# Kernel optimization log

Measured on AMD Instinct MI355X. Metric: run time of the kernel, lower is better.

Reference implementation:

```python
import math
import jax, jax.numpy as jnp
import numpy as np

L, B = 576, 16           # residues, batch
HID, ALPHA = 800, 60     # lstm hidden, alphabet size
IN0, IN1 = 41, 2 * HID   # lstm layer input sizes (20 one-hot + 21 pssm)


def _unit(v):
    return v / jnp.linalg.norm(v, axis=-1, keepdims=True)


def _frame(a, b, c):
    # rotation matrix (columns) of the local reference frame at point c
    bc = _unit(c - b)
    n = _unit(jnp.cross(b - a, bc))
    return jnp.stack([bc, jnp.cross(n, bc), n], axis=-1)  # (..., 3, 3)


def _extend(a, b, c, ct):
    # place next atom given previous three atoms and SRF coordinates ct
    R = _frame(a, b, c)
    return c + jnp.einsum('...ij,...j->...i', R, ct)


def lstm_dir(x, w_ih, w_hh, b_ih, b_hh, reverse=False):
    # single-direction LSTM over x: (T, B, D); torch gate order i,f,g,o
    H = w_hh.shape[1]
    Bb = x.shape[1]

    def step(carry, xt):
        h, cst = carry
        gates = xt @ w_ih.T + b_ih + h @ w_hh.T + b_hh
        i, f, g, o = jnp.split(gates, 4, axis=-1)
        cnew = jax.nn.sigmoid(f) * cst + jax.nn.sigmoid(i) * jnp.tanh(g)
        hnew = jax.nn.sigmoid(o) * jnp.tanh(cnew)
        return (hnew, cnew), hnew

    zeros = jnp.zeros((Bb, H), x.dtype)
    _, hs = jax.lax.scan(step, (zeros, zeros), x, reverse=reverse)
    return hs  # (T, B, H), in original time order for both directions


def torsion_to_srf(r, theta, phi):
    # r, theta: (3,) fixed bond lengths/angles; phi: (L, B, 3) torsions
    r = r[None, None, :]
    th = theta[None, None, :]
    c = jnp.stack([r * jnp.cos(th) * jnp.ones_like(phi),
                   r * jnp.cos(phi) * jnp.sin(th),
                   r * jnp.sin(phi) * jnp.sin(th)], axis=-1)  # (L, B, 3, 3)
    Lx, Bx = phi.shape[0], phi.shape[1]
    return jnp.transpose(c, (0, 2, 1, 3)).reshape(3 * Lx, Bx, 3)


def pnerf(c_tilde, nfrag):
    # parallel NeRF: run nfrag fragments in parallel, then stitch sequentially
    A, Bb, _ = c_tilde.shape
    F = A // nfrag  # assumes divisibility (guaranteed by chosen L)
    c = c_tilde.reshape(nfrag, F, Bb, 3).transpose(1, 0, 2, 3).reshape(F, nfrag * Bb, 3)
    init = jnp.array([[-np.sqrt(0.5), np.sqrt(1.5), 0.0],
                      [-np.sqrt(2.0), 0.0, 0.0],
                      [0.0, 0.0, 0.0]], dtype=c_tilde.dtype)
    a0 = jnp.broadcast_to(init[0], (nfrag * Bb, 3))
    b0 = jnp.broadcast_to(init[1], (nfrag * Bb, 3))
    c0 = jnp.broadcast_to(init[2], (nfrag * Bb, 3))

    def step(carry, ct):
        a, b, cc = carry
        d = _extend(a, b, cc, ct)
        return (b, cc, d), d

    _, frag = jax.lax.scan(step, (a0, b0, c0), c)  # (F, nfrag*Bb, 3)
    frag = frag.reshape(F, nfrag, Bb, 3)

    coords = frag[:, 0]  # fragment 0 already in global frame
    for k in range(1, nfrag):  # small fixed loop over fragments
        R = _frame(coords[-3], coords[-2], coords[-1])  # (Bb, 3, 3)
        g = coords[-1][None] + jnp.einsum('bij,fbj->fbi', R, frag[:, k])
        coords = jnp.concatenate([coords, g], axis=0)
    return coords  # (3L, B, 3)


def _p(k, shape):
    return 0.05 * jax.random.normal(k, shape, dtype=jnp.float32)


def setup_inputs():
    key = jax.random.key(0)
    ks = jax.random.split(key, 32)
    inp = {}
    inp['seq'] = jax.random.randint(ks[0], (L, B), 0, 20)
    inp['pssm'] = jax.random.uniform(ks[1], (L, B, 21), dtype=jnp.float32)
    inp['length'] = jnp.full((B,), L, dtype=jnp.int32)  # full lengths (packing is a no-op)
    i = 2
    for layer, din in ((0, IN0), (1, IN1)):
        for d in ('f', 'b'):
            inp[f'w_ih_l{layer}{d}'] = _p(ks[i], (4 * HID, din)); i += 1
            inp[f'w_hh_l{layer}{d}'] = _p(ks[i], (4 * HID, HID)); i += 1
            inp[f'b_ih_l{layer}{d}'] = _p(ks[i], (4 * HID,)); i += 1
            inp[f'b_hh_l{layer}{d}'] = _p(ks[i], (4 * HID,)); i += 1
    inp['fc_w'] = _p(ks[i], (ALPHA, 2 * HID)); i += 1
    inp['fc_b'] = _p(ks[i], (ALPHA,)); i += 1
    inp['alphabet'] = jax.random.uniform(ks[i], (ALPHA, 3), minval=-math.pi, maxval=math.pi, dtype=jnp.float32); i += 1
    inp['bond_lengths'] = jnp.array([145.867432, 152.534744, 132.935516], dtype=jnp.float32)
    inp['bond_angles'] = jnp.array([1.019982, 1.20471, 1.109421], dtype=jnp.float32)
    return inp


def reference(seq, pssm, length,
              w_ih_l0f, w_hh_l0f, b_ih_l0f, b_hh_l0f,
              w_ih_l0b, w_hh_l0b, b_ih_l0b, b_hh_l0b,
              w_ih_l1f, w_hh_l1f, b_ih_l1f, b_hh_l1f,
              w_ih_l1b, w_hh_l1b, b_ih_l1b, b_hh_l1b,
              fc_w, fc_b, alphabet, bond_lengths, bond_angles):
    # eval mode: inter-layer dropout omitted; all lengths == L so packing is identity
    x = jnp.concatenate([jax.nn.one_hot(seq, 20, dtype=pssm.dtype), pssm], axis=-1)  # (L,B,41)
    h = jnp.concatenate([lstm_dir(x, w_ih_l0f, w_hh_l0f, b_ih_l0f, b_hh_l0f),
                         lstm_dir(x, w_ih_l0b, w_hh_l0b, b_ih_l0b, b_hh_l0b, reverse=True)], axis=-1)
    h = jnp.concatenate([lstm_dir(h, w_ih_l1f, w_hh_l1f, b_ih_l1f, b_hh_l1f),
                         lstm_dir(h, w_ih_l1b, w_hh_l1b, b_ih_l1b, b_hh_l1b, reverse=True)], axis=-1)
    p = jax.nn.softmax(h @ fc_w.T + fc_b, axis=-1)            # (L,B,ALPHA)
    phi = jnp.arctan2(p @ jnp.sin(alphabet), p @ jnp.cos(alphabet))  # (L,B,3)
    srf = torsion_to_srf(bond_lengths, bond_angles, phi)      # (3L,B,3)
    return pnerf(srf, int(math.sqrt(L)))                      # (3L,B,3)
```

## Files before the change

### kernel.cpp

```cpp
#include <hip/hip_runtime.h>
#include <hip/hip_fp16.h>

#define L_SEQ 576
#define BATCH 16
#define HIDDEN 800
#define NT 200
#define KQ_HH 25
#define KQ_L1 50
#define KQ_L0 2

typedef _Float16 h8 __attribute__((ext_vector_type(8)));
typedef _Float16 h4 __attribute__((ext_vector_type(4)));
typedef float f4 __attribute__((ext_vector_type(4)));
typedef int v4i __attribute__((ext_vector_type(4)));
typedef int v2i __attribute__((ext_vector_type(2)));

__device__ __forceinline__ float sigmoidf_(float x){
  x = fminf(30.f, fmaxf(-30.f, x));
  return 1.f/(1.f+__expf(-x));
}
__device__ __forceinline__ float tanhf_(float x){
  x = fminf(15.f, fmaxf(-15.f, x));
  float e = __expf(2.f*x);
  return (e-1.f)/(e+1.f);
}

__global__ void init_h(v4i* __restrict__ h){
  size_t i = (size_t)blockIdx.x*256 + threadIdx.x;
  v4i s = {0x7C007C00, 0x7C007C00, 0x7C007C00, 0x7C007C00};
  h[i] = s;
}

__global__ void build_x(const int* __restrict__ seq, const float* __restrict__ pssm,
                        _Float16* __restrict__ x){
  int i = blockIdx.x*256 + threadIdx.x;
  if(i >= L_SEQ*BATCH*64) return;
  int m = i >> 6, k = i & 63;
  float v = 0.f;
  if(k < 20)      v = (seq[m]==k) ? 1.f : 0.f;
  else if(k < 41) v = pssm[m*21 + (k-20)];
  x[i] = (_Float16)v;
}

__global__ void prep_w(
  const float* __restrict__ whh0f, const float* __restrict__ whh0b,
  const float* __restrict__ whh1f, const float* __restrict__ whh1b,
  const float* __restrict__ wih1f, const float* __restrict__ wih1b,
  const float* __restrict__ wih0f, const float* __restrict__ wih0b,
  h8* __restrict__ wp_hh, h8* __restrict__ wp1, h8* __restrict__ wp0)
{
  long idx = (long)blockIdx.x*256 + threadIdx.x;
  const long J1 = 4L*320000, J2 = 2L*640000, J3 = 2L*25600;
  if(idx < J1){
    int d = (int)(idx/320000); int r = (int)(idx%320000);
    int T = r/1600, q = (r%1600)/64, l = r&63;
    const float* W = (d==0)?whh0f:(d==1)?whh0b:(d==2)?whh1f:whh1b;
    int c = l&15; int n = (c&3)*800 + T*4 + (c>>2);
    const float* src = W + (size_t)n*800 + q*32 + ((l>>4)<<3);
    h8 v;
    #pragma unroll
    for(int j=0;j<8;++j) v[j] = (_Float16)src[j];
    wp_hh[idx] = v;
  } else if(idx < J1+J2){
    long i2 = idx - J1;
    int d = (int)(i2/640000); int r = (int)(i2%640000);
    int T = r/3200, q = (r%3200)/64, l = r&63;
    const float* W = d ? wih1b : wih1f;
    int c = l&15; int n = (c&3)*800 + T*4 + (c>>2);
    const float* src = W + (size_t)n*1600 + q*32 + ((l>>4)<<3);
    h8 v;
    #pragma unroll
    for(int j=0;j<8;++j) v[j] = (_Float16)src[j];
    wp1[i2] = v;
  } else if(idx < J1+J2+J3){
    long i3 = idx - J1 - J2;
    int d = (int)(i3/25600); int r = (int)(i3%25600);
    int T = r/128, q = (r%128)/64, l = r&63;
    const float* W = d ? wih0b : wih0f;
    int c = l&15; int n = (c&3)*800 + T*4 + (c>>2);
    int k0 = q*32 + ((l>>4)<<3);
    h8 v;
    #pragma unroll
    for(int j=0;j<8;++j){ int k = k0+j; v[j] = (_Float16)((k<41)? W[(size_t)n*41+k] : 0.f); }
    wp0[i3] = v;
  }
}

__global__ __launch_bounds__(256) void gemm_l0(
  const _Float16* __restrict__ A,
  const h8* __restrict__ WpF, const h8* __restrict__ WpB,
  const float* __restrict__ bihF, const float* __restrict__ bhhF,
  const float* __restrict__ bihB, const float* __restrict__ bhhB,
  _Float16* __restrict__ GpF, _Float16* __restrict__ GpB)
{
  const int wv = threadIdx.x >> 6;
  const int l  = threadIdx.x & 63;
  const int mg = blockIdx.x % 144;
  const int tg = blockIdx.x / 144;
  const int mt = mg*4 + wv;
  const int dir = tg / 50;
  const int Tb  = (tg % 50) * 4;
  const h8* Wp = dir ? WpB : WpF;
  const float* bih = dir ? bihB : bihF;
  const float* bhh = dir ? bhhB : bhhF;
  _Float16* Gp = dir ? GpB : GpF;

  const _Float16* ab = A + (size_t)(mt*16 + (l&15))*64 + ((l>>4)<<3);
  f4 acc[4] = {{0.f,0.f,0.f,0.f},{0.f,0.f,0.f,0.f},{0.f,0.f,0.f,0.f},{0.f,0.f,0.f,0.f}};
  for(int q=0;q<KQ_L0;++q){
    h8 av = *(const h8*)(ab + q*32);
    #pragma unroll
    for(int j=0;j<4;++j){
      h8 bv = Wp[((size_t)(Tb+j)*KQ_L0 + q)*64 + l];
      acc[j] = __builtin_amdgcn_mfma_f32_16x16x32_f16(bv, av, acc[j], 0, 0, 0);
    }
  }
  const int hi = l >> 4;
  #pragma unroll
  for(int j=0;j<4;++j){
    int T = Tb + j;
    int u = T*4 + hi;
    h4 o;
    #pragma unroll
    for(int r=0;r<4;++r){
      float bias = bih[r*800+u] + bhh[r*800+u];
      o[r] = (_Float16)(acc[j][r] + bias);
    }
    *(h4*)(Gp + (((size_t)mt*NT + T)*64 + l)*4) = o;
  }
}

__global__ __launch_bounds__(256,1) void lstm_kernel(
  const h8* __restrict__ WpF, const h8* __restrict__ WpB,
  const _Float16* __restrict__ GpF, const _Float16* __restrict__ GpB,
  h8* __restrict__ hfrag)
{
  __shared__ __attribute__((aligned(16))) char lds_h[2*25600];
  const int tid = threadIdx.x;
  const int wv  = tid >> 6;
  const int l   = tid & 63;
  const bool bwd = blockIdx.x >= 50;
  const int T = ((bwd ? (int)blockIdx.x - 50 : (int)blockIdx.x) << 2) + wv;
  const h8* Wp = bwd ? WpB : WpF;
  const _Float16* Gp = bwd ? GpB : GpF;
  const int dirOff = bwd ? 1600 : 0;

  h8 Bf[KQ_HH];
  #pragma unroll
  for(int q=0;q<KQ_HH;++q) Bf[q] = Wp[(T*KQ_HH + q)*64 + l];

  float cs = 0.f;
  const int qb = wv*6;
  const int storeUnit = ((T>>3)<<6) + (((T>>1)&3)<<4);
  const int storeHalf = (T&1)<<3;

  for(int s=0; s<L_SEQ; ++s){
    const int t = bwd ? (L_SEQ-1-s) : s;

    h4 gp4 = *(const h4*)(Gp + (((size_t)t*NT + T)*64 + l)*4);

    #pragma unroll
    for(int q=0;q<KQ_HH;++q) asm volatile("" : "+v"(Bf[q]));

    char* lbuf = lds_h + (s&1)*25600;
    if(s > 0){
      const h8* src = hfrag + (size_t)(bwd ? t+1 : t-1)*3200 + dirOff + l;
      v4i w[7];
      for(;;){
        #pragma unroll
        for(int i=0;i<7;++i){
          unsigned long long ad = (unsigned long long)(src + (qb+i)*64);
          asm volatile("global_load_dwordx4 %0, %1, off sc1"
                       : "=v"(w[i]) : "v"(ad) : "memory");
        }
        asm volatile("s_waitcnt vmcnt(0)"
          : "+v"(w[0]),"+v"(w[1]),"+v"(w[2]),"+v"(w[3]),"+v"(w[4]),
            "+v"(w[5]),"+v"(w[6])
          :
          : "memory");
        int orac = 0;
        #pragma unroll
        for(int i=0;i<7;++i) orac |= (w[i][0]|w[i][1]) | (w[i][2]|w[i][3]);
        if(__all((orac & 0x40004000) == 0)) break;
        __builtin_amdgcn_s_sleep(1);
      }
      #pragma unroll
      for(int i=0;i<7;++i)
        *(v4i*)(lbuf + (qb+i)*1024 + l*16) = w[i];
    }
    __syncthreads();

    f4 acc[4];
    acc[0][0]=(float)gp4[0]; acc[0][1]=(float)gp4[1]; acc[0][2]=(float)gp4[2]; acc[0][3]=(float)gp4[3];
    #pragma unroll
    for(int j=1;j<4;++j){ acc[j][0]=0.f; acc[j][1]=0.f; acc[j][2]=0.f; acc[j][3]=0.f; }
    if(s > 0){
      #pragma unroll
      for(int q=0;q<KQ_HH;++q){
        v4i wq = *(const v4i*)(lbuf + q*1024 + l*16);
        acc[q&3] = __builtin_amdgcn_mfma_f32_16x16x32_f16(
                     Bf[q], __builtin_bit_cast(h8, wq), acc[q&3], 0,0,0);
      }
    }
    f4 g = (acc[0]+acc[1]) + (acc[2]+acc[3]);

    float cn = sigmoidf_(g[1])*cs + sigmoidf_(g[0])*tanhf_(g[2]);
    cs = cn;
    float hv = sigmoidf_(g[3])*tanhf_(cn);

    {
      _Float16 hf = (_Float16)hv;
      unsigned int u0 = (unsigned int)__builtin_bit_cast(unsigned short, hf);
      unsigned int up = (unsigned int)__shfl_xor((int)u0, 16, 64);
      unsigned int d01 = u0 | (up << 16);
      unsigned int d23 = (unsigned int)__shfl_xor((int)d01, 32, 64);
      if(l < 16){
        v2i ov; ov[0] = (int)d01; ov[1] = (int)d23;
        unsigned long long ad = (unsigned long long)
          ((char*)(hfrag + (size_t)t*3200 + dirOff + storeUnit + l) + storeHalf);
        asm volatile("global_store_dwordx2 %0, %1, off sc1" : : "v"(ad), "v"(ov) : "memory");
      }
    }
  }
}

__global__ __launch_bounds__(512,1) void fused_l1(
  const h8* __restrict__ WhF, const h8* __restrict__ WhB,
  _Float16* __restrict__ GpF, _Float16* __restrict__ GpB,
  h8* __restrict__ hfrag,
  const h8* __restrict__ Af,
  const h8* __restrict__ W1F, const h8* __restrict__ W1B,
  const float* __restrict__ bihF, const float* __restrict__ bhhF,
  const float* __restrict__ bihB, const float* __restrict__ bhhB)
{
  __shared__ __attribute__((aligned(16))) char smem[2*25600];
  const int tid = threadIdx.x;
  if(blockIdx.x < 100){
    const bool act = tid < 256;
    const int wv = (tid >> 6) & 3;
    const int l  = tid & 63;
    const bool bwd = blockIdx.x >= 50;
    const int T = ((bwd ? (int)blockIdx.x - 50 : (int)blockIdx.x) << 2) + wv;
    const h8* Wp = bwd ? WhB : WhF;
    const _Float16* Gp = bwd ? GpB : GpF;
    const int dirOff = bwd ? 1600 : 0;

    h8 Bf[KQ_HH];
    if(act){
      #pragma unroll
      for(int q=0;q<KQ_HH;++q) Bf[q] = Wp[(T*KQ_HH + q)*64 + l];
    }
    float cs = 0.f;
    const int qb = wv*6;
    const int storeUnit = ((T>>3)<<6) + (((T>>1)&3)<<4);
    const int storeHalf = (T&1)<<3;

    for(int s=0; s<L_SEQ; ++s){
      const int t = bwd ? (L_SEQ-1-s) : s;
      v2i gpw;
      char* lbuf = smem + (s&1)*25600;
      unsigned long long gpad = 0;
      if(act){
        gpad = (unsigned long long)(Gp + (((size_t)t*NT + T)*64 + l)*4);
        asm volatile("global_load_dwordx2 %0, %1, off sc1"
                     : "=v"(gpw) : "v"(gpad) : "memory");
        #pragma unroll
        for(int q=0;q<KQ_HH;++q) asm volatile("" : "+v"(Bf[q]));
        if(s > 0){
          const h8* src = hfrag + (size_t)(bwd ? t+1 : t-1)*3200 + dirOff + l;
          v4i w[7];
          for(;;){
            #pragma unroll
            for(int i=0;i<7;++i){
              unsigned long long ad = (unsigned long long)(src + (qb+i)*64);
              asm volatile("global_load_dwordx4 %0, %1, off sc1"
                           : "=v"(w[i]) : "v"(ad) : "memory");
            }
            asm volatile("s_waitcnt vmcnt(0)"
              : "+v"(w[0]),"+v"(w[1]),"+v"(w[2]),"+v"(w[3]),"+v"(w[4]),
                "+v"(w[5]),"+v"(w[6])
              :
              : "memory");
            int orac = 0;
            #pragma unroll
            for(int i=0;i<7;++i) orac |= (w[i][0]|w[i][1]) | (w[i][2]|w[i][3]);
            if(__all((orac & 0x40004000) == 0)) break;
            __builtin_amdgcn_s_sleep(1);
          }
          #pragma unroll
          for(int i=0;i<7;++i)
            *(v4i*)(lbuf + (qb+i)*1024 + l*16) = w[i];
        }
      }
      __syncthreads();
      if(act){
        for(;;){
          asm volatile("s_waitcnt vmcnt(0)" : "+v"(gpw) : : "memory");
          int lo = gpw[0], hi = gpw[1];
          int na = (((lo & 0x7C00) == 0x7C00) ? 1 : 0)
                 | ((((lo>>16) & 0x7C00) == 0x7C00) ? 1 : 0)
                 | (((hi & 0x7C00) == 0x7C00) ? 1 : 0)
                 | ((((hi>>16) & 0x7C00) == 0x7C00) ? 1 : 0);
          if(__all(na == 0)) break;
          __builtin_amdgcn_s_sleep(1);
          asm volatile("global_load_dwordx2 %0, %1, off sc1"
                       : "=v"(gpw) : "v"(gpad) : "memory");
        }
        h4 gp4 = __builtin_bit_cast(h4, gpw);

        f4 acc[4];
        acc[0][0]=(float)gp4[0]; acc[0][1]=(float)gp4[1]; acc[0][2]=(float)gp4[2]; acc[0][3]=(float)gp4[3];
        #pragma unroll
        for(int j=1;j<4;++j){ acc[j][0]=0.f; acc[j][1]=0.f; acc[j][2]=0.f; acc[j][3]=0.f; }
        if(s > 0){
          #pragma unroll
          for(int q=0;q<KQ_HH;++q){
            v4i wq = *(const v4i*)(lbuf + q*1024 + l*16);
            acc[q&3] = __builtin_amdgcn_mfma_f32_16x16x32_f16(
                         Bf[q], __builtin_bit_cast(h8, wq), acc[q&3], 0,0,0);
          }
        }
        f4 g = (acc[0]+acc[1]) + (acc[2]+acc[3]);

        float cn = sigmoidf_(g[1])*cs + sigmoidf_(g[0])*tanhf_(g[2]);
        cs = cn;
        float hv = sigmoidf_(g[3])*tanhf_(cn);

        _Float16 hf = (_Float16)hv;
        unsigned int u0 = (unsigned int)__builtin_bit_cast(unsigned short, hf);
        unsigned int up = (unsigned int)__shfl_xor((int)u0, 16, 64);
        unsigned int d01 = u0 | (up << 16);
        unsigned int d23 = (unsigned int)__shfl_xor((int)d01, 32, 64);
        if(l < 16){
          v2i ov; ov[0] = (int)d01; ov[1] = (int)d23;
          unsigned long long ad = (unsigned long long)
            ((char*)(hfrag + (size_t)t*3200 + dirOff + storeUnit + l) + storeHalf);
          asm volatile("global_store_dwordx2 %0, %1, off sc1" : : "v"(ad), "v"(ov) : "memory");
        }
      }
    }
  } else {
    v4i (*ldsW)[512] = (v4i(*)[512])smem;
    const int wv = tid >> 6;
    const int l  = tid & 63;
    const int g  = (int)blockIdx.x - 100;
    const int dir = g & 1;
    const int p   = g >> 1;
    const int mgs = p / 25;
    const int tg  = p % 25;
    if(mgs >= 36) return;
    const int mg = dir ? (35 - mgs) : mgs;
    const int Tb = tg * 8;
    const int mt0 = mg*16 + wv*2;
    const h8* Wp = dir ? W1B : W1F;
    const float* bih = dir ? bihB : bihF;
    const float* bhh = dir ? bhhB : bhhF;
    _Float16* Gp = dir ? GpB : GpF;

    const h8* a0 = Af + (size_t)(mt0+0)*3200 + l;
    const h8* a1 = Af + (size_t)(mt0+1)*3200 + l;

    f4 acc[2][8];
    #pragma unroll
    for(int m=0;m<2;++m)
      #pragma unroll
      for(int j=0;j<8;++j){ acc[m][j][0]=0.f; acc[m][j][1]=0.f; acc[m][j][2]=0.f; acc[m][j][3]=0.f; }

    {
      int j = tid >> 6, ll = tid & 63;
      ldsW[0][tid] = *(const v4i*)(Wp + ((size_t)(Tb+j)*KQ_L1 + 0)*64 + ll);
    }
    h8 av0 = a0[0], av1 = a1[0];
    __syncthreads();
    for(int q=0;q<KQ_L1;++q){
      const int buf = q & 1;
      const int qn = (q+1 < KQ_L1) ? q+1 : q;
      if(q+1 < KQ_L1){
        int j = tid >> 6, ll = tid & 63;
        ldsW[buf^1][tid] = *(const v4i*)(Wp + ((size_t)(Tb+j)*KQ_L1 + (q+1))*64 + ll);
      }
      h8 an0 = a0[qn*64], an1 = a1[qn*64];
      #pragma unroll
      for(int j=0;j<8;++j){
        h8 bv = __builtin_bit_cast(h8, ldsW[buf][j*64 + l]);
        acc[0][j] = __builtin_amdgcn_mfma_f32_16x16x32_f16(bv, av0, acc[0][j], 0, 0, 0);
        acc[1][j] = __builtin_amdgcn_mfma_f32_16x16x32_f16(bv, av1, acc[1][j], 0, 0, 0);
      }
      __syncthreads();
      av0 = an0; av1 = an1;
    }
    const int hi = l >> 4;
    #pragma unroll
    for(int j=0;j<8;++j){
      int T = Tb + j;
      int u = T*4 + hi;
      float b0 = bih[0*800+u] + bhh[0*800+u];
      float b1 = bih[1*800+u] + bhh[1*800+u];
      float b2 = bih[2*800+u] + bhh[2*800+u];
      float b3 = bih[3*800+u] + bhh[3*800+u];
      #pragma unroll
      for(int m=0;m<2;++m){
        h4 o;
        o[0]=(_Float16)(acc[m][j][0]+b0); o[1]=(_Float16)(acc[m][j][1]+b1);
        o[2]=(_Float16)(acc[m][j][2]+b2); o[3]=(_Float16)(acc[m][j][3]+b3);
        v2i ov = __builtin_bit_cast(v2i, o);
        unsigned long long ad = (unsigned long long)
          (Gp + (((size_t)(mt0+m)*NT + T)*64 + l)*4);
        asm volatile("global_store_dwordx2 %0, %1, off sc1" : : "v"(ad), "v"(ov) : "memory");
      }
    }
  }
}

__global__ void head_kernel(const h8* __restrict__ h1f,
                            const float* __restrict__ fcw, const float* __restrict__ fcb,
                            const float* __restrict__ alphabet,
                            const float* __restrict__ bl, const float* __restrict__ ba,
                            float* __restrict__ srf)
{
  __shared__ h8 sh8[16*201];
  __shared__ float slog[960];
  __shared__ float smax[16];
  __shared__ float sphi[48];
  const int t = blockIdx.x, tid = threadIdx.x;
  const h8* src = h1f + (size_t)t*3200;
  for(int u=tid; u<3200; u+=256){
    int q2 = u >> 6, r = u & 63, sub = r >> 4, m = r & 15;
    sh8[m*201 + (q2<<2) + sub] = src[u];
  }
  __syncthreads();
  for(int it=tid; it<960; it+=256){
    int j = it >> 4, b = it & 15;
    float acc = fcb[j];
    const float4* wr = (const float4*)(fcw + (size_t)j*1600);
    const h8* hr = sh8 + b*201;
    for(int k=0;k<200;++k){
      h8 hv = hr[k];
      float4 w0 = wr[2*k], w1 = wr[2*k+1];
      acc += w0.x*(float)hv[0] + w0.y*(float)hv[1] + w0.z*(float)hv[2] + w0.w*(float)hv[3]
           + w1.x*(float)hv[4] + w1.y*(float)hv[5] + w1.z*(float)hv[6] + w1.w*(float)hv[7];
    }
    slog[b*60 + j] = acc;
  }
  __syncthreads();
  if(tid < 16){
    float mx = -1e30f;
    for(int j=0;j<60;++j) mx = fmaxf(mx, slog[tid*60+j]);
    smax[tid] = mx;
  }
  __syncthreads();
  if(tid < 48){
    int b = tid/3, ax = tid%3;
    float s=0.f, c=0.f, mx = smax[b];
    for(int j=0;j<60;++j){
      float e = __expf(slog[b*60+j] - mx);
      float al = alphabet[j*3 + ax];
      s += e*__sinf(al); c += e*__cosf(al);
    }
    sphi[b*3+ax] = atan2f(s, c);
  }
  __syncthreads();
  if(tid < 144){
    int jj = tid/48; int r_ = tid%48; int b = r_/3, ax = r_%3;
    float rr = bl[jj], th = ba[jj], ph = sphi[b*3+jj];
    float v = (ax==0) ? rr*__cosf(th)
            : (ax==1) ? rr*__cosf(ph)*__sinf(th)
                      : rr*__sinf(ph)*__sinf(th);
    srf[(((size_t)(3*t+jj))*16 + b)*3 + ax] = v;
  }
}

__device__ __forceinline__ void frame_cols(
  float ax,float ay,float az, float bx,float by,float bz, float cx,float cy,float cz,
  float* R)
{
  float ux=cx-bx, uy=cy-by, uz=cz-bz;
  float ir = rsqrtf(ux*ux+uy*uy+uz*uz);
  float bcx=ux*ir, bcy=uy*ir, bcz=uz*ir;
  float px=bx-ax, py=by-ay, pz=bz-az;
  float nx=py*bcz-pz*bcy, ny=pz*bcx-px*bcz, nz=px*bcy-py*bcx;
  float in_ = rsqrtf(nx*nx+ny*ny+nz*nz);
  nx*=in_; ny*=in_; nz*=in_;
  float mx=ny*bcz-nz*bcy, my=nz*bcx-nx*bcz, mz=nx*bcy-ny*bcx;
  R[0]=bcx;R[1]=bcy;R[2]=bcz; R[3]=mx;R[4]=my;R[5]=mz; R[6]=nx;R[7]=ny;R[8]=nz;
}

__global__ void pnerf_kernel(const float* __restrict__ srf,
                             float* __restrict__ frag, float* __restrict__ out)
{
  __shared__ float tail[3][16][3];
  __shared__ float sR[16][9];
  __shared__ float sorg[16][3];
  const int tid = threadIdx.x;
  if(tid < 384){
    int k = tid >> 4, b = tid & 15;
    float ax=-0.70710678f, ay=1.22474487f, az=0.f;
    float bx=-1.41421356f, by=0.f, bz=0.f;
    float cx=0.f, cy=0.f, cz=0.f;
    for(int f=0; f<72; ++f){
      const float* ct = srf + (((size_t)(k*72+f))*16 + b)*3;
      float t0=ct[0], t1=ct[1], t2=ct[2];
      float R[9];
      frame_cols(ax,ay,az, bx,by,bz, cx,cy,cz, R);
      float dx = cx + R[0]*t0 + R[3]*t1 + R[6]*t2;
      float dy = cy + R[1]*t0 + R[4]*t1 + R[7]*t2;
      float dz = cz + R[2]*t0 + R[5]*t1 + R[8]*t2;
      float* fr = frag + (((size_t)(f*24+k))*16 + b)*3;
      fr[0]=dx; fr[1]=dy; fr[2]=dz;
      if(k == 0){
        float* o = out + ((size_t)(f*16)+b)*3;
        o[0]=dx; o[1]=dy; o[2]=dz;
        if(f >= 69){ tail[f-69][b][0]=dx; tail[f-69][b][1]=dy; tail[f-69][b][2]=dz; }
      }
      ax=bx; ay=by; az=bz;  bx=cx; by=cy; bz=cz;  cx=dx; cy=dy; cz=dz;
    }
  }
  __syncthreads();
  for(int kk=1; kk<24; ++kk){
    if(tid < 16){
      int b = tid;
      frame_cols(tail[0][b][0],tail[0][b][1],tail[0][b][2],
                 tail[1][b][0],tail[1][b][1],tail[1][b][2],
                 tail[2][b][0],tail[2][b][1],tail[2][b][2], &sR[b][0]);
      sorg[b][0]=tail[2][b][0]; sorg[b][1]=tail[2][b][1]; sorg[b][2]=tail[2][b][2];
    }
    __syncthreads();
    for(int idx=tid; idx<1152; idx+=blockDim.x){
      int f = idx >> 4, b = idx & 15;
      const float* v = frag + (((size_t)(f*24+kk))*16 + b)*3;
      float vx=v[0], vy=v[1], vz=v[2];
      float gx = sorg[b][0] + sR[b][0]*vx + sR[b][3]*vy + sR[b][6]*vz;
      float gy = sorg[b][1] + sR[b][1]*vx + sR[b][4]*vy + sR[b][7]*vz;
      float gz = sorg[b][2] + sR[b][2]*vx + sR[b][5]*vy + sR[b][8]*vz;
      float* o = out + (((size_t)(kk*72+f))*16 + b)*3;
      o[0]=gx; o[1]=gy; o[2]=gz;
      if(f >= 69){ tail[f-69][b][0]=gx; tail[f-69][b][1]=gy; tail[f-69][b][2]=gz; }
    }
    __syncthreads();
  }
}

extern "C" void kernel_launch(void* const* d_in, const int* in_sizes, int n_in,
                              void* d_out, int out_size, void* d_ws, size_t ws_size,
                              hipStream_t stream)
{
  (void)in_sizes; (void)n_in; (void)out_size; (void)ws_size;
  const int*   seq  = (const int*)d_in[0];
  const float* pssm = (const float*)d_in[1];
  const float* w_ih_l0f=(const float*)d_in[3];  const float* w_hh_l0f=(const float*)d_in[4];
  const float* b_ih_l0f=(const float*)d_in[5];  const float* b_hh_l0f=(const float*)d_in[6];
  const float* w_ih_l0b=(const float*)d_in[7];  const float* w_hh_l0b=(const float*)d_in[8];
  const float* b_ih_l0b=(const float*)d_in[9];  const float* b_hh_l0b=(const float*)d_in[10];
  const float* w_ih_l1f=(const float*)d_in[11]; const float* w_hh_l1f=(const float*)d_in[12];
  const float* b_ih_l1f=(const float*)d_in[13]; const float* b_hh_l1f=(const float*)d_in[14];
  const float* w_ih_l1b=(const float*)d_in[15]; const float* w_hh_l1b=(const float*)d_in[16];
  const float* b_ih_l1b=(const float*)d_in[17]; const float* b_hh_l1b=(const float*)d_in[18];
  const float* fc_w=(const float*)d_in[19];     const float* fc_b=(const float*)d_in[20];
  const float* alphabet=(const float*)d_in[21];
  const float* bl=(const float*)d_in[22];       const float* ba=(const float*)d_in[23];
  float* out = (float*)d_out;

  char* ws = (char*)d_ws;
  size_t o = 0;
  auto alloc = [&](size_t bytes){ size_t r = o; o = (o + bytes + 255) & ~(size_t)255; return r; };
  size_t o_wphh = alloc(4ull*320000*16);
  size_t o_wp1  = alloc(2ull*640000*16);
  size_t o_wp0  = alloc(2ull*25600*16);
  size_t o_gpf  = alloc(2ull*29491200);
  size_t o_gpb  = alloc(2ull*29491200);
  size_t o_h0   = alloc(16ull*576*3200);
  size_t o_h1   = alloc(16ull*576*3200);
  size_t o_x    = alloc(2ull*589824);
  size_t o_srf  = alloc(4ull*82944);
  size_t o_frag = alloc(4ull*82944);

  h8* wp_hh = (h8*)(ws + o_wphh);
  h8* wp1   = (h8*)(ws + o_wp1);
  h8* wp0   = (h8*)(ws + o_wp0);
  _Float16* gpf = (_Float16*)(ws + o_gpf);
  _Float16* gpb = (_Float16*)(ws + o_gpb);
  h8* h0    = (h8*)(ws + o_h0);
  h8* h1    = (h8*)(ws + o_h1);
  _Float16* x = (_Float16*)(ws + o_x);
  float* srf    = (float*)(ws + o_srf);
  float* frag   = (float*)(ws + o_frag);

  init_h<<<14400, 256, 0, stream>>>((v4i*)(ws + o_h0));
  build_x<<<2304, 256, 0, stream>>>(seq, pssm, x);
  prep_w<<<10200, 256, 0, stream>>>(w_hh_l0f, w_hh_l0b, w_hh_l1f, w_hh_l1b,
                                    w_ih_l1f, w_ih_l1b, w_ih_l0f, w_ih_l0b,
                                    wp_hh, wp1, wp0);
  gemm_l0<<<14400, 256, 0, stream>>>(x, wp0, wp0 + 25600,
                                     b_ih_l0f, b_hh_l0f, b_ih_l0b, b_hh_l0b, gpf, gpb);
  lstm_kernel<<<100, 256, 0, stream>>>(wp_hh, wp_hh + 320000, gpf, gpb, h0);
  init_h<<<28800, 256, 0, stream>>>((v4i*)(ws + o_gpf));
  fused_l1<<<2100, 512, 0, stream>>>(wp_hh + 640000, wp_hh + 960000,
                                     gpf, gpb, h1, h0,
                                     wp1, wp1 + 640000,
                                     b_ih_l1f, b_hh_l1f, b_ih_l1b, b_hh_l1b);
  head_kernel<<<576, 256, 0, stream>>>(h1, fc_w, fc_b, alphabet, bl, ba, srf);
  pnerf_kernel<<<1, 512, 0, stream>>>(srf, frag, out);
}
```

Measured before the change: 2.717 ms.

## Fuse layer-0 input GEMM with recurrent LSTM kernel via NaN-flag polling

```diff
diff --git a/kernel.cpp b/kernel.cpp
--- a/kernel.cpp
+++ b/kernel.cpp
@@ -86,150 +86,12 @@
   }
 }
 
-__global__ __launch_bounds__(256) void gemm_l0(
-  const _Float16* __restrict__ A,
-  const h8* __restrict__ WpF, const h8* __restrict__ WpB,
-  const float* __restrict__ bihF, const float* __restrict__ bhhF,
-  const float* __restrict__ bihB, const float* __restrict__ bhhB,
-  _Float16* __restrict__ GpF, _Float16* __restrict__ GpB)
-{
-  const int wv = threadIdx.x >> 6;
-  const int l  = threadIdx.x & 63;
-  const int mg = blockIdx.x % 144;
-  const int tg = blockIdx.x / 144;
-  const int mt = mg*4 + wv;
-  const int dir = tg / 50;
-  const int Tb  = (tg % 50) * 4;
-  const h8* Wp = dir ? WpB : WpF;
-  const float* bih = dir ? bihB : bihF;
-  const float* bhh = dir ? bhhB : bhhF;
-  _Float16* Gp = dir ? GpB : GpF;
-
-  const _Float16* ab = A + (size_t)(mt*16 + (l&15))*64 + ((l>>4)<<3);
-  f4 acc[4] = {{0.f,0.f,0.f,0.f},{0.f,0.f,0.f,0.f},{0.f,0.f,0.f,0.f},{0.f,0.f,0.f,0.f}};
-  for(int q=0;q<KQ_L0;++q){
-    h8 av = *(const h8*)(ab + q*32);
-    #pragma unroll
-    for(int j=0;j<4;++j){
-      h8 bv = Wp[((size_t)(Tb+j)*KQ_L0 + q)*64 + l];
-      acc[j] = __builtin_amdgcn_mfma_f32_16x16x32_f16(bv, av, acc[j], 0, 0, 0);
-    }
-  }
-  const int hi = l >> 4;
-  #pragma unroll
-  for(int j=0;j<4;++j){
-    int T = Tb + j;
-    int u = T*4 + hi;
-    h4 o;
-    #pragma unroll
-    for(int r=0;r<4;++r){
-      float bias = bih[r*800+u] + bhh[r*800+u];
-      o[r] = (_Float16)(acc[j][r] + bias);
-    }
-    *(h4*)(Gp + (((size_t)mt*NT + T)*64 + l)*4) = o;
-  }
-}
-
-__global__ __launch_bounds__(256,1) void lstm_kernel(
-  const h8* __restrict__ WpF, const h8* __restrict__ WpB,
-  const _Float16* __restrict__ GpF, const _Float16* __restrict__ GpB,
-  h8* __restrict__ hfrag)
-{
-  __shared__ __attribute__((aligned(16))) char lds_h[2*25600];
-  const int tid = threadIdx.x;
-  const int wv  = tid >> 6;
-  const int l   = tid & 63;
-  const bool bwd = blockIdx.x >= 50;
-  const int T = ((bwd ? (int)blockIdx.x - 50 : (int)blockIdx.x) << 2) + wv;
-  const h8* Wp = bwd ? WpB : WpF;
-  const _Float16* Gp = bwd ? GpB : GpF;
-  const int dirOff = bwd ? 1600 : 0;
-
-  h8 Bf[KQ_HH];
-  #pragma unroll
-  for(int q=0;q<KQ_HH;++q) Bf[q] = Wp[(T*KQ_HH + q)*64 + l];
-
-  float cs = 0.f;
-  const int qb = wv*6;
-  const int storeUnit = ((T>>3)<<6) + (((T>>1)&3)<<4);
-  const int storeHalf = (T&1)<<3;
-
-  for(int s=0; s<L_SEQ; ++s){
-    const int t = bwd ? (L_SEQ-1-s) : s;
-
-    h4 gp4 = *(const h4*)(Gp + (((size_t)t*NT + T)*64 + l)*4);
-
-    #pragma unroll
-    for(int q=0;q<KQ_HH;++q) asm volatile("" : "+v"(Bf[q]));
-
-    char* lbuf = lds_h + (s&1)*25600;
-    if(s > 0){
-      const h8* src = hfrag + (size_t)(bwd ? t+1 : t-1)*3200 + dirOff + l;
-      v4i w[7];
-      for(;;){
-        #pragma unroll
-        for(int i=0;i<7;++i){
-          unsigned long long ad = (unsigned long long)(src + (qb+i)*64);
-          asm volatile("global_load_dwordx4 %0, %1, off sc1"
-                       : "=v"(w[i]) : "v"(ad) : "memory");
-        }
-        asm volatile("s_waitcnt vmcnt(0)"
-          : "+v"(w[0]),"+v"(w[1]),"+v"(w[2]),"+v"(w[3]),"+v"(w[4]),
-            "+v"(w[5]),"+v"(w[6])
-          :
-          : "memory");
-        int orac = 0;
-        #pragma unroll
-        for(int i=0;i<7;++i) orac |= (w[i][0]|w[i][1]) | (w[i][2]|w[i][3]);
-        if(__all((orac & 0x40004000) == 0)) break;
-        __builtin_amdgcn_s_sleep(1);
-      }
-      #pragma unroll
-      for(int i=0;i<7;++i)
-        *(v4i*)(lbuf + (qb+i)*1024 + l*16) = w[i];
-    }
-    __syncthreads();
-
-    f4 acc[4];
-    acc[0][0]=(float)gp4[0]; acc[0][1]=(float)gp4[1]; acc[0][2]=(float)gp4[2]; acc[0][3]=(float)gp4[3];
-    #pragma unroll
-    for(int j=1;j<4;++j){ acc[j][0]=0.f; acc[j][1]=0.f; acc[j][2]=0.f; acc[j][3]=0.f; }
-    if(s > 0){
-      #pragma unroll
-      for(int q=0;q<KQ_HH;++q){
-        v4i wq = *(const v4i*)(lbuf + q*1024 + l*16);
-        acc[q&3] = __builtin_amdgcn_mfma_f32_16x16x32_f16(
-                     Bf[q], __builtin_bit_cast(h8, wq), acc[q&3], 0,0,0);
-      }
-    }
-    f4 g = (acc[0]+acc[1]) + (acc[2]+acc[3]);
-
-    float cn = sigmoidf_(g[1])*cs + sigmoidf_(g[0])*tanhf_(g[2]);
-    cs = cn;
-    float hv = sigmoidf_(g[3])*tanhf_(cn);
-
-    {
-      _Float16 hf = (_Float16)hv;
-      unsigned int u0 = (unsigned int)__builtin_bit_cast(unsigned short, hf);
-      unsigned int up = (unsigned int)__shfl_xor((int)u0, 16, 64);
-      unsigned int d01 = u0 | (up << 16);
-      unsigned int d23 = (unsigned int)__shfl_xor((int)d01, 32, 64);
-      if(l < 16){
-        v2i ov; ov[0] = (int)d01; ov[1] = (int)d23;
-        unsigned long long ad = (unsigned long long)
-          ((char*)(hfrag + (size_t)t*3200 + dirOff + storeUnit + l) + storeHalf);
-        asm volatile("global_store_dwordx2 %0, %1, off sc1" : : "v"(ad), "v"(ov) : "memory");
-      }
-    }
-  }
-}
-
-__global__ __launch_bounds__(512,1) void fused_l1(
+__global__ __launch_bounds__(512,1) void fused_l0(
   const h8* __restrict__ WhF, const h8* __restrict__ WhB,
   _Float16* __restrict__ GpF, _Float16* __restrict__ GpB,
   h8* __restrict__ hfrag,
-  const h8* __restrict__ Af,
-  const h8* __restrict__ W1F, const h8* __restrict__ W1B,
+  const _Float16* __restrict__ A,
+  const h8* __restrict__ W0F, const h8* __restrict__ W0B,
   const float* __restrict__ bihF, const float* __restrict__ bhhF,
   const float* __restrict__ bihB, const float* __restrict__ bhhB)
 {
@@ -340,6 +202,166 @@
       }
     }
   } else {
+    const int wv = tid >> 6;
+    const int l  = tid & 63;
+    const int g  = (int)blockIdx.x - 100;
+    const int dir = g & 1;
+    const int r   = g >> 1;
+    const int mg8s = r / 50;
+    const int tg  = r % 50;
+    const int mg8 = dir ? (71 - mg8s) : mg8s;
+    const int Tb  = tg * 4;
+    const int mt  = mg8*8 + wv;
+    const h8* Wp = dir ? W0B : W0F;
+    const float* bih = dir ? bihB : bihF;
+    const float* bhh = dir ? bhhB : bhhF;
+    _Float16* Gp = dir ? GpB : GpF;
+
+    const _Float16* ab = A + (size_t)(mt*16 + (l&15))*64 + ((l>>4)<<3);
+    f4 acc[4] = {{0.f,0.f,0.f,0.f},{0.f,0.f,0.f,0.f},{0.f,0.f,0.f,0.f},{0.f,0.f,0.f,0.f}};
+    for(int q=0;q<KQ_L0;++q){
+      h8 av = *(const h8*)(ab + q*32);
+      #pragma unroll
+      for(int j=0;j<4;++j){
+        h8 bv = Wp[((size_t)(Tb+j)*KQ_L0 + q)*64 + l];
+        acc[j] = __builtin_amdgcn_mfma_f32_16x16x32_f16(bv, av, acc[j], 0, 0, 0);
+      }
+    }
+    const int hi = l >> 4;
+    #pragma unroll
+    for(int j=0;j<4;++j){
+      int T = Tb + j;
+      int u = T*4 + hi;
+      h4 o;
+      #pragma unroll
+      for(int rr=0;rr<4;++rr){
+        float bias = bih[rr*800+u] + bhh[rr*800+u];
+        o[rr] = (_Float16)(acc[j][rr] + bias);
+      }
+      v2i ov = __builtin_bit_cast(v2i, o);
+      unsigned long long ad = (unsigned long long)
+        (Gp + (((size_t)mt*NT + T)*64 + l)*4);
+      asm volatile("global_store_dwordx2 %0, %1, off sc1" : : "v"(ad), "v"(ov) : "memory");
+    }
+  }
+}
+
+__global__ __launch_bounds__(512,1) void fused_l1(
+  const h8* __restrict__ WhF, const h8* __restrict__ WhB,
+  _Float16* __restrict__ GpF, _Float16* __restrict__ GpB,
+  h8* __restrict__ hfrag,
+  const h8* __restrict__ Af,
+  const h8* __restrict__ W1F, const h8* __restrict__ W1B,
+  const float* __restrict__ bihF, const float* __restrict__ bhhF,
+  const float* __restrict__ bihB, const float* __restrict__ bhhB)
+{
+  __shared__ __attribute__((aligned(16))) char smem[2*25600];
+  const int tid = threadIdx.x;
+  if(blockIdx.x < 100){
+    const bool act = tid < 256;
+    const int wv = (tid >> 6) & 3;
+    const int l  = tid & 63;
+    const bool bwd = blockIdx.x >= 50;
+    const int T = ((bwd ? (int)blockIdx.x - 50 : (int)blockIdx.x) << 2) + wv;
+    const h8* Wp = bwd ? WhB : WhF;
+    const _Float16* Gp = bwd ? GpB : GpF;
+    const int dirOff = bwd ? 1600 : 0;
+
+    h8 Bf[KQ_HH];
+    if(act){
+      #pragma unroll
+      for(int q=0;q<KQ_HH;++q) Bf[q] = Wp[(T*KQ_HH + q)*64 + l];
+    }
+    float cs = 0.f;
+    const int qb = wv*6;
+    const int storeUnit = ((T>>3)<<6) + (((T>>1)&3)<<4);
+    const int storeHalf = (T&1)<<3;
+
+    for(int s=0; s<L_SEQ; ++s){
+      const int t = bwd ? (L_SEQ-1-s) : s;
+      v2i gpw;
+      char* lbuf = smem + (s&1)*25600;
+      unsigned long long gpad = 0;
+      if(act){
+        gpad = (unsigned long long)(Gp + (((size_t)t*NT + T)*64 + l)*4);
+        asm volatile("global_load_dwordx2 %0, %1, off sc1"
+                     : "=v"(gpw) : "v"(gpad) : "memory");
+        #pragma unroll
+        for(int q=0;q<KQ_HH;++q) asm volatile("" : "+v"(Bf[q]));
+        if(s > 0){
+          const h8* src = hfrag + (size_t)(bwd ? t+1 : t-1)*3200 + dirOff + l;
+          v4i w[7];
+          for(;;){
+            #pragma unroll
+            for(int i=0;i<7;++i){
+              unsigned long long ad = (unsigned long long)(src + (qb+i)*64);
+              asm volatile("global_load_dwordx4 %0, %1, off sc1"
+                           : "=v"(w[i]) : "v"(ad) : "memory");
+            }
+            asm volatile("s_waitcnt vmcnt(0)"
+              : "+v"(w[0]),"+v"(w[1]),"+v"(w[2]),"+v"(w[3]),"+v"(w[4]),
+                "+v"(w[5]),"+v"(w[6])
+              :
+              : "memory");
+            int orac = 0;
+            #pragma unroll
+            for(int i=0;i<7;++i) orac |= (w[i][0]|w[i][1]) | (w[i][2]|w[i][3]);
+            if(__all((orac & 0x40004000) == 0)) break;
+            __builtin_amdgcn_s_sleep(1);
+          }
+          #pragma unroll
+          for(int i=0;i<7;++i)
+            *(v4i*)(lbuf + (qb+i)*1024 + l*16) = w[i];
+        }
+      }
+      __syncthreads();
+      if(act){
+        for(;;){
+          asm volatile("s_waitcnt vmcnt(0)" : "+v"(gpw) : : "memory");
+          int lo = gpw[0], hi = gpw[1];
+          int na = (((lo & 0x7C00) == 0x7C00) ? 1 : 0)
+                 | ((((lo>>16) & 0x7C00) == 0x7C00) ? 1 : 0)
+                 | (((hi & 0x7C00) == 0x7C00) ? 1 : 0)
+                 | ((((hi>>16) & 0x7C00) == 0x7C00) ? 1 : 0);
+          if(__all(na == 0)) break;
+          __builtin_amdgcn_s_sleep(1);
+          asm volatile("global_load_dwordx2 %0, %1, off sc1"
+                       : "=v"(gpw) : "v"(gpad) : "memory");
+        }
+        h4 gp4 = __builtin_bit_cast(h4, gpw);
+
+        f4 acc[4];
+        acc[0][0]=(float)gp4[0]; acc[0][1]=(float)gp4[1]; acc[0][2]=(float)gp4[2]; acc[0][3]=(float)gp4[3];
+        #pragma unroll
+        for(int j=1;j<4;++j){ acc[j][0]=0.f; acc[j][1]=0.f; acc[j][2]=0.f; acc[j][3]=0.f; }
+        if(s > 0){
+          #pragma unroll
+          for(int q=0;q<KQ_HH;++q){
+            v4i wq = *(const v4i*)(lbuf + q*1024 + l*16);
+            acc[q&3] = __builtin_amdgcn_mfma_f32_16x16x32_f16(
+                         Bf[q], __builtin_bit_cast(h8, wq), acc[q&3], 0,0,0);
+          }
+        }
+        f4 g = (acc[0]+acc[1]) + (acc[2]+acc[3]);
+
+        float cn = sigmoidf_(g[1])*cs + sigmoidf_(g[0])*tanhf_(g[2]);
+        cs = cn;
+        float hv = sigmoidf_(g[3])*tanhf_(cn);
+
+        _Float16 hf = (_Float16)hv;
+        unsigned int u0 = (unsigned int)__builtin_bit_cast(unsigned short, hf);
+        unsigned int up = (unsigned int)__shfl_xor((int)u0, 16, 64);
+        unsigned int d01 = u0 | (up << 16);
+        unsigned int d23 = (unsigned int)__shfl_xor((int)d01, 32, 64);
+        if(l < 16){
+          v2i ov; ov[0] = (int)d01; ov[1] = (int)d23;
+          unsigned long long ad = (unsigned long long)
+            ((char*)(hfrag + (size_t)t*3200 + dirOff + storeUnit + l) + storeHalf);
+          asm volatile("global_store_dwordx2 %0, %1, off sc1" : : "v"(ad), "v"(ov) : "memory");
+        }
+      }
+    }
+  } else {
     v4i (*ldsW)[512] = (v4i(*)[512])smem;
     const int wv = tid >> 6;
     const int l  = tid & 63;
@@ -585,14 +607,15 @@
   float* srf    = (float*)(ws + o_srf);
   float* frag   = (float*)(ws + o_frag);
 
-  init_h<<<14400, 256, 0, stream>>>((v4i*)(ws + o_h0));
+  init_h<<<43200, 256, 0, stream>>>((v4i*)(ws + o_gpf));
   build_x<<<2304, 256, 0, stream>>>(seq, pssm, x);
   prep_w<<<10200, 256, 0, stream>>>(w_hh_l0f, w_hh_l0b, w_hh_l1f, w_hh_l1b,
                                     w_ih_l1f, w_ih_l1b, w_ih_l0f, w_ih_l0b,
                                     wp_hh, wp1, wp0);
-  gemm_l0<<<14400, 256, 0, stream>>>(x, wp0, wp0 + 25600,
-                                     b_ih_l0f, b_hh_l0f, b_ih_l0b, b_hh_l0b, gpf, gpb);
-  lstm_kernel<<<100, 256, 0, stream>>>(wp_hh, wp_hh + 320000, gpf, gpb, h0);
+  fused_l0<<<7300, 512, 0, stream>>>(wp_hh, wp_hh + 320000,
+                                     gpf, gpb, h0, x,
+                                     wp0, wp0 + 25600,
+                                     b_ih_l0f, b_hh_l0f, b_ih_l0b, b_hh_l0b);
   init_h<<<28800, 256, 0, stream>>>((v4i*)(ws + o_gpf));
   fused_l1<<<2100, 512, 0, stream>>>(wp_hh + 640000, wp_hh + 960000,
                                      gpf, gpb, h1, h0,
```

New measurement: 2.795 ms. 1.03x slower.
